# Optimization experiments

Measured on AMD Instinct MI355X. Metric: run time of the kernel, lower is better.

## Reference

```python
import jax, jax.numpy as jnp
import numpy as np

DIM = 1536
NH = 12
HD = DIM // NH  # 128
F_, H_, W_ = 16, 16, 16
L = F_ * H_ * W_  # 4096


def _precompute_freqs(dim, max_positions, base=10000.0):
    # [max_positions, dim//2] angles
    half = dim // 2
    inv = 1.0 / base ** (np.arange(0, half * 2, 2, dtype=np.float32) / (half * 2))
    pos = np.arange(max_positions, dtype=np.float32)
    return pos[:, None] * inv[None, :]


def _get_3d_freqs(head_dim, F, H, W, base=10000.0):
    half_hd = head_dim // 2
    n_t = max(1, head_dim // 4 // 2)
    n_h = max(1, head_dim * 3 // 8 // 2)
    n_w = half_hd - n_t - n_h
    ft = _precompute_freqs(n_t * 2, F, base)  # [F, n_t]
    fh = _precompute_freqs(n_h * 2, H, base)  # [H, n_h]
    fw = _precompute_freqs(n_w * 2, W, base)  # [W, n_w]
    f_idx = np.broadcast_to(ft[:, None, None, :], (F, H, W, n_t))
    h_idx = np.broadcast_to(fh[None, :, None, :], (F, H, W, n_h))
    w_idx = np.broadcast_to(fw[None, None, :, :], (F, H, W, n_w))
    return np.concatenate([f_idx, h_idx, w_idx], axis=-1).reshape(F * H * W, half_hd)


def setup_inputs() -> dict:
    key = jax.random.key(0)
    ks = jax.random.split(key, 9)
    s = 1.0 / np.sqrt(DIM)
    x = jax.random.normal(ks[0], (1, L, DIM), dtype=jnp.float32)
    freqs = jnp.asarray(_get_3d_freqs(HD, F_, H_, W_), dtype=jnp.float32)
    Wq = jax.random.normal(ks[1], (DIM, DIM), dtype=jnp.float32) * s
    bq = jax.random.normal(ks[2], (DIM,), dtype=jnp.float32) * 0.01
    Wk = jax.random.normal(ks[3], (DIM, DIM), dtype=jnp.float32) * s
    bk = jax.random.normal(ks[4], (DIM,), dtype=jnp.float32) * 0.01
    Wv = jax.random.normal(ks[5], (DIM, DIM), dtype=jnp.float32) * s
    bv = jax.random.normal(ks[6], (DIM,), dtype=jnp.float32) * 0.01
    Wo = jax.random.normal(ks[7], (DIM, DIM), dtype=jnp.float32) * s
    bo = jax.random.normal(ks[8], (DIM,), dtype=jnp.float32) * 0.01
    return {"x": x, "freqs": freqs, "Wq": Wq, "bq": bq, "Wk": Wk, "bk": bk,
            "Wv": Wv, "bv": bv, "Wo": Wo, "bo": bo}


def _apply_rotary(t, cos_v, sin_v):
    # t: [B, Nh, L, Hd]; cos_v/sin_v: [L, Hd//2]
    B, Nh, Lq, Hd = t.shape
    t2 = t.reshape(B, Nh, Lq, Hd // 2, 2)
    x0, x1 = t2[..., 0], t2[..., 1]
    r0 = x0 * cos_v - x1 * sin_v
    r1 = x0 * sin_v + x1 * cos_v
    return jnp.stack([r0, r1], axis=-1).reshape(B, Nh, Lq, Hd)


def reference(x, freqs, Wq, bq, Wk, bk, Wv, bv, Wo, bo):
    B, Lq, D = x.shape
    Nh, Hd = NH, D // NH
    q = (x @ Wq + bq).reshape(B, Lq, Nh, Hd).transpose(0, 2, 1, 3)
    k = (x @ Wk + bk).reshape(B, Lq, Nh, Hd).transpose(0, 2, 1, 3)
    v = (x @ Wv + bv).reshape(B, Lq, Nh, Hd).transpose(0, 2, 1, 3)
    cos_v = jnp.cos(freqs)  # [L, Hd//2]
    sin_v = jnp.sin(freqs)
    q = _apply_rotary(q, cos_v, sin_v)
    k = _apply_rotary(k, cos_v, sin_v)
    scale = 1.0 / jnp.sqrt(jnp.asarray(Hd, dtype=x.dtype))
    scores = jnp.einsum('bhqd,bhkd->bhqk', q, k) * scale
    attn = jax.nn.softmax(scores, axis=-1)
    out = jnp.einsum('bhqk,bhkd->bhqd', attn, v)
    out = out.transpose(0, 2, 1, 3).reshape(B, Lq, D)
    return out @ Wo + bo
```

## Files before the change

### kernel.cpp

```cpp
#include <hip/hip_runtime.h>

#define DIM 1536
#define NH  12
#define HD  128
#define SEQ 4096

typedef unsigned short u16;
typedef unsigned int   u32;
typedef __attribute__((ext_vector_type(8))) short bf16x8;
typedef __attribute__((ext_vector_type(4))) float f32x4;
typedef __attribute__((ext_vector_type(16))) float f32x16;

static __device__ __forceinline__ u16 f2bf(float f) {
    u32 u = __float_as_uint(f);
    u32 r = u + 0x7FFFu + ((u >> 16) & 1u);
    return (u16)(r >> 16);
}
static __device__ __forceinline__ u32 pack2(float a, float b) {
    return (u32)f2bf(a) | ((u32)f2bf(b) << 16);
}

#define GLL(g, s) __builtin_amdgcn_global_load_lds( \
    (const __attribute__((address_space(1))) void*)(g), \
    (__attribute__((address_space(3))) void*)(s), 16, 0, 0)

#define SCLQ 0.127532f

__global__ __launch_bounds__(256) void k_cvt_x(const float* __restrict__ x, u16* __restrict__ xb) {
    int gid = blockIdx.x * 256 + threadIdx.x;
    const float4* p = (const float4*)x + (size_t)gid * 2;
    float4 a = p[0], b = p[1];
    uint4 o;
    o.x = pack2(a.x, a.y); o.y = pack2(a.z, a.w);
    o.z = pack2(b.x, b.y); o.w = pack2(b.z, b.w);
    *(uint4*)(xb + (size_t)gid * 8) = o;
}

__global__ __launch_bounds__(256) void k_transpose_w(const float* __restrict__ Wq, const float* __restrict__ Wk,
                                                     const float* __restrict__ Wv, const float* __restrict__ Wo,
                                                     u16* __restrict__ wqkv, u16* __restrict__ wot) {
    __shared__ float tile[32][33];
    int z = blockIdx.z;
    const float* W = z == 0 ? Wq : z == 1 ? Wk : z == 2 ? Wv : Wo;
    u16* out = z < 3 ? (wqkv + (size_t)z * DIM * DIM) : wot;
    int tx = threadIdx.x, ty = threadIdx.y;
    int c0 = blockIdx.x * 32, r0 = blockIdx.y * 32;
#pragma unroll
    for (int i = 0; i < 4; i++)
        tile[ty + i * 8][tx] = W[(size_t)(r0 + ty + i * 8) * DIM + c0 + tx];
    __syncthreads();
#pragma unroll
    for (int i = 0; i < 4; i++)
        out[(size_t)(c0 + ty + i * 8) * DIM + r0 + tx] = f2bf(tile[tx][ty + i * 8]);
}

__global__ __launch_bounds__(256) void k_prep(const float* __restrict__ fr, const float* __restrict__ bq,
                                              const float* __restrict__ bk, const float* __restrict__ bv,
                                              float2* __restrict__ cs, float* __restrict__ bqkv) {
    int gid = blockIdx.x * 256 + threadIdx.x;
    float f = fr[gid];
    cs[gid] = make_float2(cosf(f), sinf(f));
    if (gid < 3 * DIM)
        bqkv[gid] = gid < DIM ? bq[gid] : gid < 2 * DIM ? bk[gid - DIM] : bv[gid - 2 * DIM];
}

__global__ __launch_bounds__(256, 3) void k_gemm(const u16* __restrict__ A, const u16* __restrict__ B,
                                                 const float* __restrict__ bias, int Kdim, int mode,
                                                 const float2* __restrict__ cs2,
                                                 u16* __restrict__ qo, u16* __restrict__ ko,
                                                 u16* __restrict__ vto, float* __restrict__ outf) {
    __shared__ u16 As[2][128 * 32];
    __shared__ u16 Bs[2][192 * 32];
    const int tid = threadIdx.x;
    const int w = tid >> 6, l = tid & 63;
    const int wr = w >> 1, wc = w & 1;
    const int lr = l & 15, lg = l >> 4;
    int nwg = gridDim.x * gridDim.y;
    int bid = blockIdx.y * gridDim.x + blockIdx.x;
    int swz = (bid & 7) * (nwg >> 3) + (bid >> 3);
    const int m0 = (swz / gridDim.x) * 128, n0 = (swz % gridDim.x) * 192;
    f32x4 acc[4][6] = {};

    const int srow = l >> 2;
    const int scol = (((l & 3) * 16) ^ (((l >> 2) & 3) << 4)) >> 1;
    const size_t Ab0 = (size_t)(m0 + (w * 2 + 0) * 16 + srow) * Kdim + scol;
    const size_t Ab1 = (size_t)(m0 + (w * 2 + 1) * 16 + srow) * Kdim + scol;
    const size_t Bb0 = (size_t)(n0 + (w * 3 + 0) * 16 + srow) * Kdim + scol;
    const size_t Bb1 = (size_t)(n0 + (w * 3 + 1) * 16 + srow) * Kdim + scol;
    const size_t Bb2 = (size_t)(n0 + (w * 3 + 2) * 16 + srow) * Kdim + scol;
    const int ao0 = (w * 2 + 0) * 512, ao1 = (w * 2 + 1) * 512;
    const int bo0 = (w * 3 + 0) * 512, bo1 = (w * 3 + 1) * 512, bo2 = (w * 3 + 2) * 512;

#define STAGE(buf, kt) do { \
        GLL(A + Ab0 + (kt), As[buf] + ao0); \
        GLL(A + Ab1 + (kt), As[buf] + ao1); \
        GLL(B + Bb0 + (kt), Bs[buf] + bo0); \
        GLL(B + Bb1 + (kt), Bs[buf] + bo1); \
        GLL(B + Bb2 + (kt), Bs[buf] + bo2); \
    } while (0)

    const int nk = Kdim >> 5;
    STAGE(0, 0);
    __syncthreads();

    int cur = 0;
    for (int t = 0; t < nk; ++t) {
        if (t + 1 < nk) STAGE(cur ^ 1, (t + 1) << 5);
        const u16* Ac = As[cur];
        const u16* Bc = Bs[cur];
        const int co = (lg * 8) ^ ((lr & 3) << 3);
        bf16x8 af[4], bg[6];
#pragma unroll
        for (int i = 0; i < 4; i++)
            af[i] = *(const bf16x8*)(Ac + (wr * 64 + i * 16 + lr) * 32 + co);
#pragma unroll
        for (int j = 0; j < 6; j++)
            bg[j] = *(const bf16x8*)(Bc + (wc * 96 + j * 16 + lr) * 32 + co);
#pragma unroll
        for (int i = 0; i < 4; i++)
#pragma unroll
            for (int j = 0; j < 6; j++)
                acc[i][j] = __builtin_amdgcn_mfma_f32_16x16x32_bf16(af[i], bg[j], acc[i][j], 0, 0, 0);
        __syncthreads();
        cur ^= 1;
    }
#undef STAGE

#pragma unroll
    for (int j = 0; j < 6; j++) {
        int gc = n0 + wc * 96 + j * 16 + lr;
        float bb = bias[gc];
#pragma unroll
        for (int i = 0; i < 4; i++) {
            int gr0 = m0 + wr * 64 + i * 16 + lg * 4;
            if (mode == 0) {
                int t = gc / DIM;
                int rr = gc % DIM;
                int hh = rr >> 7, hd = rr & 127;
                if (t == 2) {
                    u16* dst = vto + ((size_t)hh * HD + hd) * SEQ + gr0;
                    ushort4 pk;
                    pk.x = f2bf(acc[i][j][0] + bb);
                    pk.y = f2bf(acc[i][j][1] + bb);
                    pk.z = f2bf(acc[i][j][2] + bb);
                    pk.w = f2bf(acc[i][j][3] + bb);
                    *(ushort4*)dst = pk;
                } else {
                    bool odd = gc & 1;
                    u16* dst = (t == 0 ? qo : ko) + (size_t)hh * SEQ * HD + hd;
                    const float2* cp = cs2 + (hd >> 1);
#pragma unroll
                    for (int r = 0; r < 4; r++) {
                        float v = acc[i][j][r] + bb;
                        float vp = __shfl_xor(v, 1);
                        float2 c = cp[(size_t)(gr0 + r) * 64];
                        float o = odd ? fmaf(vp, c.y, v * c.x)
                                      : fmaf(v, c.x, -vp * c.y);
                        if (t == 0) o *= SCLQ;
                        dst[(size_t)(gr0 + r) * HD] = f2bf(o);
                    }
                }
            } else {
#pragma unroll
                for (int r = 0; r < 4; r++)
                    outf[(size_t)(gr0 + r) * DIM + gc] = acc[i][j][r] + bb;
            }
        }
    }
}

__global__ __launch_bounds__(256, 3) void k_attn(const u16* __restrict__ qb, const u16* __restrict__ kbuf,
                                                 const u16* __restrict__ vt, u16* __restrict__ attnb) {
    __shared__ u16 Ks[64 * 128];
    __shared__ u16 Vs[128 * 64];
    __shared__ float MB[128][18];
    const int tid = threadIdx.x;
    const int w = tid >> 6, l = tid & 63;
    const int qh = w & 1, kh = w >> 1;
    const int g = l >> 5, qlane = l & 31;
    const int lr = l & 15, lg = l >> 4;
    int bid = blockIdx.x;
    int gw = (bid & 7) * 96 + (bid >> 3);
    const int h = gw >> 6;
    const int q0 = (gw & 63) << 6;
    const size_t hb = (size_t)h * SEQ * HD;
    constexpr float THR = 5.0f;

    const int vrow8 = l >> 3;
    const int vc0 = (((l & 7) * 16) ^ (vrow8 << 4)) >> 1;

    bf16x8 qf[8];
    {
        const u16* qp = qb + hb + (size_t)(q0 + qh * 32 + qlane) * HD + g * 8;
#pragma unroll
        for (int s = 0; s < 8; s++)
            qf[s] = *(const bf16x8*)(qp + s * 16);
    }
    f32x16 O[4] = {};
    float m_run = -1e30f, lsum = 0.f;

    const int krow = kh * 32 + qlane;
    const int ksw = (krow & 7) << 4;
    const int vswl = (qlane & 7) << 4;

    for (int kt = 0; kt < SEQ; kt += 64) {
        __syncthreads();
#pragma unroll
        for (int c = 0; c < 4; c++) {
            int cc = w * 4 + c;
            int key = cc * 4 + lg;
            int kd0 = ((lr * 16) ^ ((key & 7) << 4)) >> 1;
            GLL(kbuf + hb + (size_t)(kt + key) * HD + kd0, Ks + cc * 512);
            int dd = cc * 8 + vrow8;
            GLL(vt + hb + (size_t)dd * SEQ + kt + vc0, Vs + cc * 512);
        }
        __syncthreads();

        f32x16 ST = {};
        const u16* Kp = Ks + krow * 128;
#pragma unroll
        for (int s = 0; s < 8; s++) {
            bf16x8 kf = *(const bf16x8*)(Kp + (((s * 32 + g * 16) ^ ksw) >> 1));
            ST = __builtin_amdgcn_mfma_f32_32x32x16_bf16(kf, qf[s], ST, 0, 0, 0);
        }

        float mx = ST[0];
#pragma unroll
        for (int r = 1; r < 16; r++) mx = fmaxf(mx, ST[r]);
        mx = fmaxf(mx, __shfl_xor(mx, 32));
        bool grow = mx > m_run + THR;
        float m_new = grow ? mx : m_run;
        if (__any(grow)) {
            float alpha = grow ? __builtin_amdgcn_exp2f(m_run - m_new) : 1.0f;
            lsum *= alpha;
            m_run = m_new;
#pragma unroll
            for (int db = 0; db < 4; db++)
#pragma unroll
                for (int r = 0; r < 16; r++) O[db][r] *= alpha;
        }
        float ps = 0.f;
#pragma unroll
        for (int r = 0; r < 16; r++) {
            float p = __builtin_amdgcn_exp2f(ST[r] - m_new);
            ST[r] = p; ps += p;
        }
        lsum += ps;

        u32 pw[2][4];
#pragma unroll
        for (int s2 = 0; s2 < 2; s2++) {
            int rb = s2 * 8;
            u32 a, b2, c2, d2;
            asm("v_cvt_pk_bf16_f32 %0, %1, %2" : "=v"(a)  : "v"(ST[rb + 0]), "v"(ST[rb + 1]));
            asm("v_cvt_pk_bf16_f32 %0, %1, %2" : "=v"(b2) : "v"(ST[rb + 2]), "v"(ST[rb + 3]));
            asm("v_cvt_pk_bf16_f32 %0, %1, %2" : "=v"(c2) : "v"(ST[rb + 4]), "v"(ST[rb + 5]));
            asm("v_cvt_pk_bf16_f32 %0, %1, %2" : "=v"(d2) : "v"(ST[rb + 6]), "v"(ST[rb + 7]));
            asm("v_permlane32_swap_b32 %0, %1" : "+v"(a), "+v"(c2));
            asm("v_permlane32_swap_b32 %0, %1" : "+v"(b2), "+v"(d2));
            pw[s2][0] = a; pw[s2][1] = b2; pw[s2][2] = c2; pw[s2][3] = d2;
        }

#pragma unroll
        for (int s2 = 0; s2 < 2; s2++) {
            union { u32 u[4]; bf16x8 v; } pf;
            pf.u[0] = pw[s2][0]; pf.u[1] = pw[s2][1]; pf.u[2] = pw[s2][2]; pf.u[3] = pw[s2][3];
            int kb2 = kh * 64 + s2 * 32 + g * 16;
#pragma unroll
            for (int db = 0; db < 4; db++) {
                int d = db * 32 + qlane;
                bf16x8 vf = *(const bf16x8*)(Vs + d * 64 + ((kb2 ^ vswl) >> 1));
                O[db] = __builtin_amdgcn_mfma_f32_32x32x16_bf16(vf, pf.v, O[db], 0, 0, 0);
            }
        }
    }

    lsum += __shfl_xor(lsum, 32);

    const int row = qh * 64 + l;
    u16* op = attnb + (size_t)(q0 + qh * 32 + qlane) * DIM + h * HD;
    __syncthreads();
    if (kh == 1) { MB[row][16] = m_run; MB[row][17] = lsum; }
    __syncthreads();
    float a0 = 0.f, a1 = 0.f;
    if (kh == 0) {
        float m1 = MB[row][16], l1 = MB[row][17];
        float mM = fmaxf(m_run, m1);
        a0 = __builtin_amdgcn_exp2f(m_run - mM);
        a1 = __builtin_amdgcn_exp2f(m1 - mM);
        float linv = 1.0f / (lsum * a0 + l1 * a1);
        a0 *= linv; a1 *= linv;
    }
#pragma unroll
    for (int db = 0; db < 4; db++) {
        __syncthreads();
        if (kh == 1) {
#pragma unroll
            for (int r = 0; r < 16; r++) MB[row][r] = O[db][r];
        }
        __syncthreads();
        if (kh == 0) {
#pragma unroll
            for (int r = 0; r < 16; r++) {
                int d = db * 32 + (r & 3) + 8 * (r >> 2) + 4 * g;
                op[d] = f2bf(O[db][r] * a0 + MB[row][r] * a1);
            }
        }
    }
}

extern "C" void kernel_launch(void* const* d_in, const int* in_sizes, int n_in,
                              void* d_out, int out_size, void* d_ws, size_t ws_size,
                              hipStream_t stream) {
    (void)in_sizes; (void)n_in; (void)out_size; (void)ws_size;
    const float* x  = (const float*)d_in[0];
    const float* fr = (const float*)d_in[1];
    const float* Wq = (const float*)d_in[2];
    const float* bq = (const float*)d_in[3];
    const float* Wk = (const float*)d_in[4];
    const float* bk = (const float*)d_in[5];
    const float* Wv = (const float*)d_in[6];
    const float* bv = (const float*)d_in[7];
    const float* Wo = (const float*)d_in[8];
    const float* bo = (const float*)d_in[9];
    float* out = (float*)d_out;

    char* ws = (char*)d_ws;
    size_t off = 0;
    auto alloc = [&](size_t b) { char* p = ws + off; off = (off + b + 255) & ~(size_t)255; return p; };
    u16*   xb    = (u16*)alloc((size_t)SEQ * DIM * 2);
    u16*   wqkv  = (u16*)alloc((size_t)3 * DIM * DIM * 2);
    u16*   wot   = (u16*)alloc((size_t)DIM * DIM * 2);
    float* bqkv  = (float*)alloc((size_t)3 * DIM * 4);
    u16*   qb    = (u16*)alloc((size_t)SEQ * DIM * 2);
    u16*   kb    = (u16*)alloc((size_t)SEQ * DIM * 2);
    u16*   vtb   = (u16*)alloc((size_t)SEQ * DIM * 2);
    u16*   attnb = (u16*)alloc((size_t)SEQ * DIM * 2);
    float2* cs   = (float2*)alloc((size_t)SEQ * 64 * 8);

    k_cvt_x<<<3072, 256, 0, stream>>>(x, xb);
    k_transpose_w<<<dim3(48, 48, 4), dim3(32, 8), 0, stream>>>(Wq, Wk, Wv, Wo, wqkv, wot);
    k_prep<<<1024, 256, 0, stream>>>(fr, bq, bk, bv, cs, bqkv);
    k_gemm<<<dim3(24, 32), 256, 0, stream>>>(xb, wqkv, bqkv, DIM, 0, cs, qb, kb, vtb, nullptr);
    k_attn<<<768, 256, 0, stream>>>(qb, kb, vtb, attnb);
    k_gemm<<<dim3(8, 32), 256, 0, stream>>>(attnb, wot, bo, DIM, 1, nullptr, nullptr, nullptr, nullptr, out);
}
```

Baseline: 259.4 us.

## Load K directly to registers and double-buffer V in LDS for attention

```diff
diff --git a/kernel.cpp b/kernel.cpp
--- a/kernel.cpp
+++ b/kernel.cpp
@@ -171,14 +171,12 @@
 
 __global__ __launch_bounds__(256, 3) void k_attn(const u16* __restrict__ qb, const u16* __restrict__ kbuf,
                                                  const u16* __restrict__ vt, u16* __restrict__ attnb) {
-    __shared__ u16 Ks[64 * 128];
-    __shared__ u16 Vs[128 * 64];
-    __shared__ float MB[128][18];
+    __shared__ u16 Vs[2][128 * 64];
+    __shared__ float MB[64][18];
     const int tid = threadIdx.x;
     const int w = tid >> 6, l = tid & 63;
     const int qh = w & 1, kh = w >> 1;
     const int g = l >> 5, qlane = l & 31;
-    const int lr = l & 15, lg = l >> 4;
     int bid = blockIdx.x;
     int gw = (bid & 7) * 96 + (bid >> 3);
     const int h = gw >> 6;
@@ -188,6 +186,7 @@
 
     const int vrow8 = l >> 3;
     const int vc0 = (((l & 7) * 16) ^ (vrow8 << 4)) >> 1;
+    const int vswl = (qlane & 7) << 4;
 
     bf16x8 qf[8];
     {
@@ -200,29 +199,41 @@
     float m_run = -1e30f, lsum = 0.f;
 
     const int krow = kh * 32 + qlane;
-    const int ksw = (krow & 7) << 4;
-    const int vswl = (qlane & 7) << 4;
-
-    for (int kt = 0; kt < SEQ; kt += 64) {
-        __syncthreads();
-#pragma unroll
-        for (int c = 0; c < 4; c++) {
-            int cc = w * 4 + c;
-            int key = cc * 4 + lg;
-            int kd0 = ((lr * 16) ^ ((key & 7) << 4)) >> 1;
-            GLL(kbuf + hb + (size_t)(kt + key) * HD + kd0, Ks + cc * 512);
-            int dd = cc * 8 + vrow8;
-            GLL(vt + hb + (size_t)dd * SEQ + kt + vc0, Vs + cc * 512);
-        }
-        __syncthreads();
+    const u16* kp = kbuf + hb + (size_t)krow * HD + g * 8;
+    bf16x8 kf[8];
+
+#define STAGEV(buf, kt) do { _Pragma("unroll") \
+    for (int c = 0; c < 4; c++) { \
+        int cc = w * 4 + c; \
+        int dd = cc * 8 + vrow8; \
+        GLL(vt + hb + (size_t)dd * SEQ + (kt) + vc0, Vs[buf] + cc * 512); \
+    } } while (0)
+#define LOADK(kt) do { const u16* kpt_ = kp + (size_t)(kt) * HD; _Pragma("unroll") \
+    for (int s = 0; s < 8; s++) kf[s] = *(const bf16x8*)(kpt_ + s * 16); \
+    } while (0)
+
+    const int NT = SEQ / 64;
+    STAGEV(0, 0);
+    LOADK(0);
+
+    for (int it = 0; it < NT; ++it) {
+        const u16* Vc = Vs[it & 1];
+        if (it + 1 < NT) {
+            STAGEV((it + 1) & 1, (it + 1) * 64);
+            asm volatile("s_waitcnt vmcnt(12)" ::: "memory");
+        } else {
+            asm volatile("s_waitcnt vmcnt(8)" ::: "memory");
+        }
+        __builtin_amdgcn_sched_barrier(0);
+        __builtin_amdgcn_s_barrier();
+        asm volatile("" ::: "memory");
 
         f32x16 ST = {};
-        const u16* Kp = Ks + krow * 128;
-#pragma unroll
-        for (int s = 0; s < 8; s++) {
-            bf16x8 kf = *(const bf16x8*)(Kp + (((s * 32 + g * 16) ^ ksw) >> 1));
-            ST = __builtin_amdgcn_mfma_f32_32x32x16_bf16(kf, qf[s], ST, 0, 0, 0);
-        }
+#pragma unroll
+        for (int s = 0; s < 8; s++)
+            ST = __builtin_amdgcn_mfma_f32_32x32x16_bf16(kf[s], qf[s], ST, 0, 0, 0);
+
+        if (it + 1 < NT) LOADK((it + 1) * 64);
 
         float mx = ST[0];
 #pragma unroll
@@ -269,41 +280,49 @@
 #pragma unroll
             for (int db = 0; db < 4; db++) {
                 int d = db * 32 + qlane;
-                bf16x8 vf = *(const bf16x8*)(Vs + d * 64 + ((kb2 ^ vswl) >> 1));
+                bf16x8 vf = *(const bf16x8*)(Vc + d * 64 + ((kb2 ^ vswl) >> 1));
                 O[db] = __builtin_amdgcn_mfma_f32_32x32x16_bf16(vf, pf.v, O[db], 0, 0, 0);
             }
         }
-    }
+
+        asm volatile("" ::: "memory");
+        __builtin_amdgcn_s_barrier();
+        asm volatile("" ::: "memory");
+    }
+#undef STAGEV
+#undef LOADK
 
     lsum += __shfl_xor(lsum, 32);
 
-    const int row = qh * 64 + l;
     u16* op = attnb + (size_t)(q0 + qh * 32 + qlane) * DIM + h * HD;
-    __syncthreads();
-    if (kh == 1) { MB[row][16] = m_run; MB[row][17] = lsum; }
-    __syncthreads();
     float a0 = 0.f, a1 = 0.f;
-    if (kh == 0) {
-        float m1 = MB[row][16], l1 = MB[row][17];
-        float mM = fmaxf(m_run, m1);
-        a0 = __builtin_amdgcn_exp2f(m_run - mM);
-        a1 = __builtin_amdgcn_exp2f(m1 - mM);
-        float linv = 1.0f / (lsum * a0 + l1 * a1);
-        a0 *= linv; a1 *= linv;
-    }
-#pragma unroll
-    for (int db = 0; db < 4; db++) {
+#pragma unroll
+    for (int qq = 0; qq < 2; ++qq) {
         __syncthreads();
-        if (kh == 1) {
-#pragma unroll
-            for (int r = 0; r < 16; r++) MB[row][r] = O[db][r];
-        }
+        if (kh == 1 && qh == qq) { MB[l][16] = m_run; MB[l][17] = lsum; }
         __syncthreads();
-        if (kh == 0) {
-#pragma unroll
-            for (int r = 0; r < 16; r++) {
-                int d = db * 32 + (r & 3) + 8 * (r >> 2) + 4 * g;
-                op[d] = f2bf(O[db][r] * a0 + MB[row][r] * a1);
+        if (kh == 0 && qh == qq) {
+            float m1 = MB[l][16], l1 = MB[l][17];
+            float mM = fmaxf(m_run, m1);
+            a0 = __builtin_amdgcn_exp2f(m_run - mM);
+            a1 = __builtin_amdgcn_exp2f(m1 - mM);
+            float linv = 1.0f / (lsum * a0 + l1 * a1);
+            a0 *= linv; a1 *= linv;
+        }
+#pragma unroll
+        for (int db = 0; db < 4; db++) {
+            __syncthreads();
+            if (kh == 1 && qh == qq) {
+#pragma unroll
+                for (int r = 0; r < 16; r++) MB[l][r] = O[db][r];
+            }
+            __syncthreads();
+            if (kh == 0 && qh == qq) {
+#pragma unroll
+                for (int r = 0; r < 16; r++) {
+                    int d = db * 32 + (r & 3) + 8 * (r >> 2) + 4 * g;
+                    op[d] = f2bf(O[db][r] * a0 + MB[l][r] * a1);
+                }
             }
         }
     }
```

Result: slower. 386.0 us (+48.8%).
